# Kernel optimization log

Hardware: AMD Instinct MI355X
Metric: run time of the kernel (lower is better)

## Reference

```python
import jax, jax.numpy as jnp
import numpy as np

N = 100000   # nodes
E = 800000   # edges
IN = 64      # in_channels
H = 128      # hidden_channels (Embedding_Dimension)
K = 9        # Num_TCN clusters
EPS = 1e-15


def setup_inputs() -> dict:
    key = jax.random.key(0)
    k0, k1, k2, k3, k4 = jax.random.split(key, 5)
    x = jax.random.normal(k0, (N, IN), jnp.float32)
    edge_index = jax.random.randint(k1, (2, E), 0, N, dtype=jnp.int32)
    batch = jnp.zeros((N,), jnp.int32)  # single graph
    W1 = jax.random.normal(k2, (IN, H), jnp.float32) / np.sqrt(IN)
    b1 = jnp.zeros((H,), jnp.float32)
    Wp = jax.random.normal(k3, (H, K), jnp.float32) / np.sqrt(H)
    bp = jax.random.normal(k4, (K,), jnp.float32) * 0.01
    return {"x": x, "edge_index": edge_index, "batch": batch,
            "W1": W1, "b1": b1, "Wp": Wp, "bp": bp}


def gcn_conv(x, edge_index, W, b):
    # GCNConv: h = D^{-1/2} (A + I) D^{-1/2} (x W) + b
    n = x.shape[0]
    h = x @ W  # [N, H]
    loop = jnp.arange(n, dtype=edge_index.dtype)
    row = jnp.concatenate([edge_index[0], loop])  # source
    col = jnp.concatenate([edge_index[1], loop])  # target
    deg = jax.ops.segment_sum(jnp.ones_like(col, jnp.float32), col, n)
    dinv = jax.lax.rsqrt(jnp.maximum(deg, 1.0))  # deg >= 1 (self loops)
    norm = dinv[row] * dinv[col]  # [E+N]
    agg = jax.ops.segment_sum(norm[:, None] * h[row], col, n)  # scatter-add at targets
    return agg + b


def reference(x, edge_index, batch, W1, b1, Wp, bp):
    n = x.shape[0]
    src, dst = edge_index[0], edge_index[1]

    hx = jax.nn.relu(gcn_conv(x, edge_index, W1, b1))  # [N, H]
    s_logits = hx @ Wp + bp                             # [N, K]
    s = jax.nn.softmax(s_logits, axis=-1)

    # pooled features and adjacency: S^T X, S^T A S (A sparse via edge list)
    x_pool = s.T @ hx                                   # [K, H]
    out_adj = jnp.einsum('ek,el->kl', s[src], s[dst])   # [K, K]

    # mincut loss: -Tr(S^T A S) / Tr(S^T D S)
    mincut_num = jnp.trace(out_adj)
    deg_a = jax.ops.segment_sum(jnp.ones((src.shape[0],), jnp.float32), dst, n)
    mincut_den = jnp.sum(deg_a * jnp.sum(s * s, axis=-1))
    mc = -(mincut_num / (mincut_den + EPS))

    # orthogonality loss: || S^T S / ||S^T S||_F - I/sqrt(K) ||_F
    ss = s.T @ s
    o = jnp.linalg.norm(ss / jnp.linalg.norm(ss) - jnp.eye(K, dtype=s.dtype) / jnp.sqrt(jnp.float32(K)))

    # normalize pooled adjacency: zero diag, symmetric degree normalization
    oa = out_adj * (1.0 - jnp.eye(K, dtype=out_adj.dtype))
    d = jnp.sum(oa, axis=-1)
    dis = jax.lax.rsqrt(d + EPS)
    oa = dis[:, None] * oa * dis[None, :]

    out = jax.nn.log_softmax(x_pool[None], axis=-1)     # [1, K, H]
    return out, mc, o, s, oa[None]
```

## Files before the change

kernel.cpp:

```cpp
#include <hip/hip_runtime.h>
#include <hip/hip_bf16.h>

#define NN 100000
#define NE 800000
#define INC 64
#define HID 128
#define KC 9
#define NBKT 782
#define BCAP 2048
#define LDA 72
#define LDH 132

#define G_XP 0
#define G_OA 1152
#define G_SS 1233
#define G_DEN 1314

typedef __attribute__((ext_vector_type(8))) short bfrag;
typedef __attribute__((ext_vector_type(4))) float facc4;

__device__ __forceinline__ float atomAddG(float* p, float v) {
  return unsafeAtomicAdd(p, v);
}

__device__ __forceinline__ unsigned short bf16rn(float x) {
  unsigned u = __float_as_uint(x);
  return (unsigned short)((u + 0x7fffu + ((u >> 16) & 1u)) >> 16);
}

__device__ __forceinline__ float bf2f(unsigned s) {
  return __uint_as_float(s << 16);
}

__device__ __forceinline__ void acc8(float wt, uint4 rv, float* acc) {
  acc[0] = fmaf(wt, bf2f(rv.x & 0xffffu), acc[0]);
  acc[1] = fmaf(wt, bf2f(rv.x >> 16), acc[1]);
  acc[2] = fmaf(wt, bf2f(rv.y & 0xffffu), acc[2]);
  acc[3] = fmaf(wt, bf2f(rv.y >> 16), acc[3]);
  acc[4] = fmaf(wt, bf2f(rv.z & 0xffffu), acc[4]);
  acc[5] = fmaf(wt, bf2f(rv.z >> 16), acc[5]);
  acc[6] = fmaf(wt, bf2f(rv.w & 0xffffu), acc[6]);
  acc[7] = fmaf(wt, bf2f(rv.w >> 16), acc[7]);
}


__global__ __launch_bounds__(256) void k_binA(const int* __restrict__ src, const int* __restrict__ dst,
                                              const float* __restrict__ W1, const float* __restrict__ Wp,
                                              const float* __restrict__ x,
                                              int* __restrict__ bcur, int* __restrict__ ebuf,
                                              unsigned short* __restrict__ W1Thi,
                                              unsigned short* __restrict__ W1Tlo,
                                              float* __restrict__ wpsT,
                                              unsigned short* __restrict__ xb) {
  int t = threadIdx.x;
  if (blockIdx.x >= 129) {
    int idx = (blockIdx.x - 129) * 256 + t;
    for (int i = idx; i < NN * 8; i += 64 * 256) {
      float4 a = ((const float4*)x)[2 * i];
      float4 b = ((const float4*)x)[2 * i + 1];
      uint4 o;
      o.x = (unsigned)bf16rn(a.x) | ((unsigned)bf16rn(a.y) << 16);
      o.y = (unsigned)bf16rn(a.z) | ((unsigned)bf16rn(a.w) << 16);
      o.z = (unsigned)bf16rn(b.x) | ((unsigned)bf16rn(b.y) << 16);
      o.w = (unsigned)bf16rn(b.z) | ((unsigned)bf16rn(b.w) << 16);
      ((uint4*)xb)[i] = o;
    }
    return;
  }
  if (blockIdx.x == 128) {
    for (int i = t; i < (INC * HID) / 4; i += 256) {
      int k = i >> 5, c4 = (i & 31) * 4;
      float4 v = ((const float4*)W1)[i];
      float vv[4] = {v.x, v.y, v.z, v.w};
#pragma unroll
      for (int j = 0; j < 4; ++j) {
        unsigned short h = bf16rn(vv[j]);
        float lo = vv[j] - __uint_as_float((unsigned)h << 16);
        W1Thi[(c4 + j) * 64 + k] = h;
        W1Tlo[(c4 + j) * 64 + k] = bf16rn(lo);
      }
    }
    for (int i = t; i < KC * HID; i += 256) {
      int q = i >> 7, c = i & 127;
      wpsT[i] = Wp[c * KC + q];
    }
    return;
  }
  __shared__ int hist[NBKT];
  __shared__ int hbase[NBKT];
  for (int b = t; b < NBKT; b += 256) hist[b] = 0;
  __syncthreads();
  int beg = blockIdx.x * 6250, end = beg + 6250;
  for (int i = beg + t; i < end; i += 256) atomicAdd(&hist[dst[i] >> 7], 1);
  __syncthreads();
  for (int b = t; b < NBKT; b += 256) {
    int h = hist[b];
    hbase[b] = h ? atomicAdd(&bcur[b], h) : 0;
    hist[b] = 0;
  }
  __syncthreads();
  for (int i = beg + t; i < end; i += 256) {
    int d = dst[i], s = src[i];
    int b = d >> 7;
    int r = atomicAdd(&hist[b], 1);
    ebuf[(size_t)b * BCAP + hbase[b] + r] = s | ((d & 127) << 17);
  }
}

__global__ __launch_bounds__(256) void k_scanb(const int* __restrict__ bcur, int* __restrict__ bbase) {
  __shared__ int sc[1024];
  int t = threadIdx.x;
  for (int i = t; i < 1024; i += 256) sc[i] = (i < NBKT) ? bcur[i] : 0;
  __syncthreads();
  for (int off = 1; off < 1024; off <<= 1) {
    int v0 = (t >= off) ? sc[t - off] : 0;
    int v1 = (t + 256 >= off) ? sc[t + 256 - off] : 0;
    int v2 = (t + 512 >= off) ? sc[t + 512 - off] : 0;
    int v3 = (t + 768 >= off) ? sc[t + 768 - off] : 0;
    __syncthreads();
    sc[t] += v0; sc[t + 256] += v1; sc[t + 512] += v2; sc[t + 768] += v3;
    __syncthreads();
  }
  for (int i = t; i < NBKT; i += 256) bbase[i] = sc[i] - bcur[i];
}

__global__ __launch_bounds__(256) void k_fillB(const int* __restrict__ bcur, const int* __restrict__ bbase,
                                               const int* __restrict__ ebuf, int* __restrict__ rowptr,
                                               int* __restrict__ degi, float* __restrict__ dinv,
                                               int* __restrict__ csr) {
  __shared__ int cnt[128], loc[128], lcur[128];
  int b = blockIdx.x;
  int t = threadIdx.x;
  if (t < 128) cnt[t] = 0;
  __syncthreads();
  int n = bcur[b];
  const int* eb = ebuf + (size_t)b * BCAP;
  for (int i = t; i < n; i += 256) atomicAdd(&cnt[eb[i] >> 17], 1);
  __syncthreads();
  if (t < 128) loc[t] = cnt[t];
  __syncthreads();
  for (int off = 1; off < 128; off <<= 1) {
    int u = (t >= off && t < 128) ? loc[t - off] : 0;
    __syncthreads();
    if (t < 128) loc[t] += u;
    __syncthreads();
  }
  int gbase = bbase[b];
  if (t < 128) {
    int node = (b << 7) + t;
    int rp = gbase + loc[t] - cnt[t];
    if (node < NN) {
      rowptr[node] = rp;
      degi[node] = cnt[t];
      dinv[node] = rsqrtf((float)cnt[t] + 1.f);
    }
    lcur[t] = rp;
  }
  __syncthreads();
  for (int i = t; i < n; i += 256) {
    int pack = eb[i];
    int s = pack & 0x1FFFF;
    int dl = pack >> 17;
    int p = atomicAdd(&lcur[dl], 1);
    csr[p] = s;
  }
}


__global__ __launch_bounds__(256) void k_gather(const int* __restrict__ rowptr, const int* __restrict__ degi,
                                                const int* __restrict__ csr,
                                                const unsigned short* __restrict__ xb,
                                                const float* __restrict__ dinv, float* __restrict__ agg) {
  int t = threadIdx.x;
  int wave = t >> 6, lane = t & 63;
  int gw = blockIdx.x * 4 + wave;
  int ng = lane >> 3, c8 = lane & 7;
  int node = gw * 8 + ng;
  if (node >= NN) return;

  float dv = dinv[node];
  int base = rowptr[node];
  int cnt = degi[node];

  float acc[8];
  {
    uint4 v = *(const uint4*)(xb + (size_t)node * 64 + c8 * 8);
    float dv2 = dv * dv;
    acc[0] = dv2 * bf2f(v.x & 0xffffu); acc[1] = dv2 * bf2f(v.x >> 16);
    acc[2] = dv2 * bf2f(v.y & 0xffffu); acc[3] = dv2 * bf2f(v.y >> 16);
    acc[4] = dv2 * bf2f(v.z & 0xffffu); acc[5] = dv2 * bf2f(v.z >> 16);
    acc[6] = dv2 * bf2f(v.w & 0xffffu); acc[7] = dv2 * bf2f(v.w >> 16);
  }

  int j = 0;
  for (; j + 3 < cnt; j += 4) {
    int s0 = csr[base + j], s1 = csr[base + j + 1], s2 = csr[base + j + 2], s3 = csr[base + j + 3];
    float w0 = dinv[s0] * dv, w1 = dinv[s1] * dv, w2 = dinv[s2] * dv, w3 = dinv[s3] * dv;
    uint4 r0 = *(const uint4*)(xb + (size_t)s0 * 64 + c8 * 8);
    uint4 r1 = *(const uint4*)(xb + (size_t)s1 * 64 + c8 * 8);
    uint4 r2 = *(const uint4*)(xb + (size_t)s2 * 64 + c8 * 8);
    uint4 r3 = *(const uint4*)(xb + (size_t)s3 * 64 + c8 * 8);
    acc8(w0, r0, acc);
    acc8(w1, r1, acc);
    acc8(w2, r2, acc);
    acc8(w3, r3, acc);
  }
  for (; j < cnt; ++j) {
    int si = csr[base + j];
    float wq = dinv[si] * dv;
    uint4 rq = *(const uint4*)(xb + (size_t)si * 64 + c8 * 8);
    acc8(wq, rq, acc);
  }
  float* ao = agg + (size_t)node * INC + c8 * 8;
  *(float4*)ao = make_float4(acc[0], acc[1], acc[2], acc[3]);
  *(float4*)(ao + 4) = make_float4(acc[4], acc[5], acc[6], acc[7]);
}


__global__ __launch_bounds__(256, 2) void k_mlpA(const float* __restrict__ agg,
                                                 const unsigned short* __restrict__ W1Thi,
                                                 const unsigned short* __restrict__ W1Tlo,
                                                 const float* __restrict__ wpsT_g,
                                                 const float* __restrict__ b1, const float* __restrict__ bp,
                                                 float* __restrict__ s_out, float* __restrict__ s_pad,
                                                 float* __restrict__ pool_part) {
  __shared__ char smem[78336];
  short* Ahi = (short*)smem;
  short* Alo = Ahi + 128 * LDA;
  short* Whi = Alo + 128 * LDA;
  short* Wlo = Whi + 128 * LDA;
  float* Hs = (float*)smem;
  float* s_lds = Hs + 128 * LDH;
  float* wpsT = (float*)(smem + 73728);

  int t = threadIdx.x;
  int nbase = blockIdx.x * 128;

#pragma unroll
  for (int j = 0; j < 8; ++j) {
    int task = t + 256 * j;
    int n = task >> 4, kq = (task & 15) * 4;
    float4 v = make_float4(0.f, 0.f, 0.f, 0.f);
    if (nbase + n < NN) v = *(const float4*)(agg + (size_t)(nbase + n) * INC + kq);
    unsigned short h0 = bf16rn(v.x), h1 = bf16rn(v.y), h2 = bf16rn(v.z), h3 = bf16rn(v.w);
    float l0f = v.x - __uint_as_float((unsigned)h0 << 16);
    float l1f = v.y - __uint_as_float((unsigned)h1 << 16);
    float l2f = v.z - __uint_as_float((unsigned)h2 << 16);
    float l3f = v.w - __uint_as_float((unsigned)h3 << 16);
    unsigned short q0 = bf16rn(l0f), q1 = bf16rn(l1f), q2 = bf16rn(l2f), q3 = bf16rn(l3f);
    *(uint2*)&Ahi[n * LDA + kq] = make_uint2((unsigned)h0 | ((unsigned)h1 << 16),
                                             (unsigned)h2 | ((unsigned)h3 << 16));
    *(uint2*)&Alo[n * LDA + kq] = make_uint2((unsigned)q0 | ((unsigned)q1 << 16),
                                             (unsigned)q2 | ((unsigned)q3 << 16));
  }
#pragma unroll
  for (int j = 0; j < 8; ++j) {
    int task = t + 256 * j;
    int c = task >> 4, k4 = (task & 15) * 4;
    *(uint2*)&Whi[c * LDA + k4] = *(const uint2*)&W1Thi[c * 64 + k4];
    *(uint2*)&Wlo[c * LDA + k4] = *(const uint2*)&W1Tlo[c * 64 + k4];
  }
  for (int i = t; i < KC * HID; i += 256) wpsT[i] = wpsT_g[i];
  __syncthreads();

  int w = t >> 6, l = t & 63;
  int r0 = w * 32;
  int lrow = l & 15;
  int lk = (l >> 4) * 8;
  int rg = (l >> 4) * 4;

  facc4 acc[2][8];
#pragma unroll
  for (int mt = 0; mt < 2; ++mt)
#pragma unroll
    for (int nt = 0; nt < 8; ++nt) acc[mt][nt] = (facc4){0.f, 0.f, 0.f, 0.f};

#pragma unroll
  for (int ks = 0; ks < 2; ++ks) {
    int ko = ks * 32 + lk;
    bfrag a0h = *(const bfrag*)&Ahi[(r0 + lrow) * LDA + ko];
    bfrag a0l = *(const bfrag*)&Alo[(r0 + lrow) * LDA + ko];
    bfrag a1h = *(const bfrag*)&Ahi[(r0 + 16 + lrow) * LDA + ko];
    bfrag a1l = *(const bfrag*)&Alo[(r0 + 16 + lrow) * LDA + ko];
#pragma unroll
    for (int nt = 0; nt < 8; ++nt) {
      bfrag bh = *(const bfrag*)&Whi[(nt * 16 + lrow) * LDA + ko];
      bfrag bl = *(const bfrag*)&Wlo[(nt * 16 + lrow) * LDA + ko];
      acc[0][nt] = __builtin_amdgcn_mfma_f32_16x16x32_bf16(a0l, bh, acc[0][nt], 0, 0, 0);
      acc[0][nt] = __builtin_amdgcn_mfma_f32_16x16x32_bf16(a0h, bl, acc[0][nt], 0, 0, 0);
      acc[0][nt] = __builtin_amdgcn_mfma_f32_16x16x32_bf16(a0h, bh, acc[0][nt], 0, 0, 0);
      acc[1][nt] = __builtin_amdgcn_mfma_f32_16x16x32_bf16(a1l, bh, acc[1][nt], 0, 0, 0);
      acc[1][nt] = __builtin_amdgcn_mfma_f32_16x16x32_bf16(a1h, bl, acc[1][nt], 0, 0, 0);
      acc[1][nt] = __builtin_amdgcn_mfma_f32_16x16x32_bf16(a1h, bh, acc[1][nt], 0, 0, 0);
    }
  }
  __syncthreads();

#pragma unroll
  for (int nt = 0; nt < 8; ++nt) {
    float b1v = b1[nt * 16 + lrow];
#pragma unroll
    for (int mt = 0; mt < 2; ++mt)
#pragma unroll
      for (int r = 0; r < 4; ++r)
        Hs[(r0 + mt * 16 + rg + r) * LDH + nt * 16 + lrow] =
            fmaxf(acc[mt][nt][r] + b1v, 0.f);
  }
  __syncthreads();

  {
    int node = t >> 1, half = t & 1;
    const float4* hrow = (const float4*)(Hs + node * LDH + half * 64);
    float4 h4[16];
#pragma unroll
    for (int cc = 0; cc < 16; ++cc) h4[cc] = hrow[cc];

    float lg[KC];
#pragma unroll
    for (int q = 0; q < KC; ++q) {
      const float4* w4 = (const float4*)(wpsT + q * HID + half * 64);
      float s0 = 0.f, s1 = 0.f, s2 = 0.f, s3 = 0.f;
#pragma unroll
      for (int cc = 0; cc < 16; ++cc) {
        float4 wv = w4[cc];
        s0 = fmaf(h4[cc].x, wv.x, s0);
        s1 = fmaf(h4[cc].y, wv.y, s1);
        s2 = fmaf(h4[cc].z, wv.z, s2);
        s3 = fmaf(h4[cc].w, wv.w, s3);
      }
      lg[q] = (s0 + s1) + (s2 + s3);
    }
#pragma unroll
    for (int q = 0; q < KC; ++q)
      lg[q] = lg[q] + __shfl_xor(lg[q], 1, 64) + bp[q];

    float m = lg[0];
#pragma unroll
    for (int q = 1; q < KC; ++q) m = fmaxf(m, lg[q]);
    float Z = 0.f;
#pragma unroll
    for (int q = 0; q < KC; ++q) { lg[q] = __expf(lg[q] - m); Z += lg[q]; }
    float inv = 1.0f / Z;
#pragma unroll
    for (int q = 0; q < KC; ++q) lg[q] *= inv;

    float4* sl = (float4*)(s_lds + node * 12);
    int gnode = nbase + node;
    if (half == 0) {
      sl[0] = make_float4(lg[0], lg[1], lg[2], lg[3]);
      if (gnode < NN) {
        ((float4*)(s_pad + (size_t)gnode * 12))[0] = make_float4(lg[0], lg[1], lg[2], lg[3]);
        float* so = s_out + (size_t)gnode * KC;
        so[0] = lg[0]; so[1] = lg[1]; so[2] = lg[2]; so[3] = lg[3]; so[4] = lg[4];
      }
    } else {
      sl[1] = make_float4(lg[4], lg[5], lg[6], lg[7]);
      s_lds[node * 12 + 8] = lg[8];
      if (gnode < NN) {
        ((float4*)(s_pad + (size_t)gnode * 12))[1] = make_float4(lg[4], lg[5], lg[6], lg[7]);
        ((float4*)(s_pad + (size_t)gnode * 12))[2] = make_float4(lg[8], 0.f, 0.f, 0.f);
        float* so = s_out + (size_t)gnode * KC;
        so[5] = lg[5]; so[6] = lg[6]; so[7] = lg[7]; so[8] = lg[8];
      }
    }
  }
  __syncthreads();

  {
    int c = t & 127, nh = t >> 7;
    float pool[KC];
#pragma unroll
    for (int q = 0; q < KC; ++q) pool[q] = 0.f;
    int lim = NN - nbase - nh * 64;
    if (lim > 64) lim = 64;
    for (int i = 0; i < lim; ++i) {
      int node = nh * 64 + i;
      float4 sa = *(const float4*)(s_lds + node * 12);
      float4 sb = *(const float4*)(s_lds + node * 12 + 4);
      float s8 = s_lds[node * 12 + 8];
      float h = Hs[node * LDH + c];
      pool[0] = fmaf(sa.x, h, pool[0]);
      pool[1] = fmaf(sa.y, h, pool[1]);
      pool[2] = fmaf(sa.z, h, pool[2]);
      pool[3] = fmaf(sa.w, h, pool[3]);
      pool[4] = fmaf(sb.x, h, pool[4]);
      pool[5] = fmaf(sb.y, h, pool[5]);
      pool[6] = fmaf(sb.z, h, pool[6]);
      pool[7] = fmaf(sb.w, h, pool[7]);
      pool[8] = fmaf(s8, h, pool[8]);
    }
    float* pp = pool_part + (size_t)(blockIdx.x * 2 + nh) * (KC * HID);
#pragma unroll
    for (int q = 0; q < KC; ++q) pp[q * HID + c] = pool[q];
  }
}


__global__ __launch_bounds__(256) void k_ssden(const float* __restrict__ s_pad,
                                               const int* __restrict__ degi,
                                               const float* __restrict__ pool_part,
                                               float* __restrict__ glob) {
  int t = threadIdx.x;
  int tid = blockIdx.x * 256 + t;
  int stride = gridDim.x * 256;

  {
    float a0 = 0.f, a1 = 0.f, a2 = 0.f, a3 = 0.f, a4 = 0.f;
    for (int p = blockIdx.x; p < 2 * NBKT; p += gridDim.x) {
      const float* row = pool_part + (size_t)p * (KC * HID);
      a0 += row[t];
      a1 += row[t + 256];
      a2 += row[t + 512];
      a3 += row[t + 768];
      if (t < 128) a4 += row[t + 1024];
    }
    atomAddG(&glob[G_XP + t], a0);
    atomAddG(&glob[G_XP + t + 256], a1);
    atomAddG(&glob[G_XP + t + 512], a2);
    atomAddG(&glob[G_XP + t + 768], a3);
    if (t < 128) atomAddG(&glob[G_XP + t + 1024], a4);
  }

  float acc[81];
  float den = 0.f;
#pragma unroll
  for (int i = 0; i < 81; ++i) acc[i] = 0.f;

  for (int node = tid; node < NN; node += stride) {
    const float4* sn = (const float4*)(s_pad + (size_t)node * 12);
    float4 a = sn[0], b = sn[1], c = sn[2];
    float s[9] = {a.x, a.y, a.z, a.w, b.x, b.y, b.z, b.w, c.x};
    float dg = (float)degi[node];
    float nrm = 0.f;
#pragma unroll
    for (int i = 0; i < 9; ++i) nrm = fmaf(s[i], s[i], nrm);
    den = fmaf(dg, nrm, den);
#pragma unroll
    for (int i = 0; i < 9; ++i)
#pragma unroll
      for (int j = 0; j < 9; ++j) acc[i * 9 + j] = fmaf(s[i], s[j], acc[i * 9 + j]);
  }

  __shared__ float wsum[4][82];
#pragma unroll
  for (int i = 0; i < 81; ++i) {
#pragma unroll
    for (int off = 32; off > 0; off >>= 1) acc[i] += __shfl_xor(acc[i], off, 64);
  }
#pragma unroll
  for (int off = 32; off > 0; off >>= 1) den += __shfl_xor(den, off, 64);
  int wave = t >> 6, lane = t & 63;
  if (lane == 0) {
#pragma unroll
    for (int i = 0; i < 81; ++i) wsum[wave][i] = acc[i];
    wsum[wave][81] = den;
  }
  __syncthreads();
  if (t < 81) atomAddG(&glob[G_SS + t], wsum[0][t] + wsum[1][t] + wsum[2][t] + wsum[3][t]);
  if (t == 81) atomAddG(&glob[G_DEN], wsum[0][81] + wsum[1][81] + wsum[2][81] + wsum[3][81]);
}


__global__ __launch_bounds__(256) void k_adj(const int* __restrict__ rowptr, const int* __restrict__ degi,
                                             const int* __restrict__ csr, const float* __restrict__ s_pad,
                                             float* __restrict__ oa_g) {
  int t = threadIdx.x;
  int tid = blockIdx.x * blockDim.x + t;
  int stride = gridDim.x * blockDim.x;

  float acc[81];
#pragma unroll
  for (int i = 0; i < 81; ++i) acc[i] = 0.f;

  for (int node = tid; node < NN; node += stride) {
    int base = rowptr[node];
    int cnt = degi[node];
    float4 g0 = make_float4(0.f, 0.f, 0.f, 0.f);
    float4 g1 = g0;
    float g8 = 0.f;
    int j = 0;
    for (; j + 1 < cnt; j += 2) {
      int s0 = csr[base + j], s1 = csr[base + j + 1];
      const float4* p0 = (const float4*)(s_pad + (size_t)s0 * 12);
      const float4* p1 = (const float4*)(s_pad + (size_t)s1 * 12);
      float4 a0 = p0[0], b0 = p0[1], c0 = p0[2];
      float4 a1 = p1[0], b1 = p1[1], c1 = p1[2];
      g0.x += a0.x + a1.x; g0.y += a0.y + a1.y; g0.z += a0.z + a1.z; g0.w += a0.w + a1.w;
      g1.x += b0.x + b1.x; g1.y += b0.y + b1.y; g1.z += b0.z + b1.z; g1.w += b0.w + b1.w;
      g8 += c0.x + c1.x;
    }
    if (j < cnt) {
      int s0 = csr[base + j];
      const float4* p0 = (const float4*)(s_pad + (size_t)s0 * 12);
      float4 a0 = p0[0], b0 = p0[1], c0 = p0[2];
      g0.x += a0.x; g0.y += a0.y; g0.z += a0.z; g0.w += a0.w;
      g1.x += b0.x; g1.y += b0.y; g1.z += b0.z; g1.w += b0.w;
      g8 += c0.x;
    }
    const float4* sn = (const float4*)(s_pad + (size_t)node * 12);
    float4 d0 = sn[0], d1 = sn[1], d2 = sn[2];
    float gg[9] = {g0.x, g0.y, g0.z, g0.w, g1.x, g1.y, g1.z, g1.w, g8};
    float sd[9] = {d0.x, d0.y, d0.z, d0.w, d1.x, d1.y, d1.z, d1.w, d2.x};
#pragma unroll
    for (int i = 0; i < 9; ++i)
#pragma unroll
      for (int jj = 0; jj < 9; ++jj) acc[i * 9 + jj] = fmaf(gg[i], sd[jj], acc[i * 9 + jj]);
  }

  __shared__ float wsum[4][81];
#pragma unroll
  for (int i = 0; i < 81; ++i) {
#pragma unroll
    for (int off = 32; off > 0; off >>= 1) acc[i] += __shfl_xor(acc[i], off, 64);
  }
  int wave = t >> 6, lane = t & 63;
  if (lane == 0) {
#pragma unroll
    for (int i = 0; i < 81; ++i) wsum[wave][i] = acc[i];
  }
  __syncthreads();
  if (t < 81) atomAddG(&oa_g[t], wsum[0][t] + wsum[1][t] + wsum[2][t] + wsum[3][t]);
}


__global__ __launch_bounds__(128) void k_final(const float* __restrict__ glob, float* __restrict__ out) {
  const float* xp = glob + G_XP;
  const float* oa = glob + G_OA;
  const float* ssm = glob + G_SS;
  const float* den = glob + G_DEN;
  int t = threadIdx.x;
  __shared__ float red[128];

  for (int k = 0; k < 9; ++k) {
    float v = xp[k * 128 + t];
    red[t] = v;
    __syncthreads();
    for (int s2 = 64; s2 > 0; s2 >>= 1) {
      if (t < s2) red[t] = fmaxf(red[t], red[t + s2]);
      __syncthreads();
    }
    float m = red[0];
    __syncthreads();
    red[t] = expf(v - m);
    __syncthreads();
    for (int s2 = 64; s2 > 0; s2 >>= 1) {
      if (t < s2) red[t] += red[t + s2];
      __syncthreads();
    }
    float lz = logf(red[0]) + m;
    __syncthreads();
    out[k * 128 + t] = v - lz;
  }

  if (t == 0) {
    float num = 0.f;
    for (int q = 0; q < 9; ++q) num += oa[q * 9 + q];
    out[1152] = -(num / (den[0] + 1e-15f));

    float fn = 0.f;
    for (int i = 0; i < 81; ++i) fn += ssm[i] * ssm[i];
    float rfn = 1.0f / sqrtf(fn);
    float osum = 0.f;
    for (int i = 0; i < 9; ++i)
      for (int j = 0; j < 9; ++j) {
        float v = ssm[i * 9 + j] * rfn - ((i == j) ? (1.0f / 3.0f) : 0.f);
        osum += v * v;
      }
    out[1153] = sqrtf(osum);
  }

  __shared__ float dsh[9];
  if (t < 9) {
    float d = 0.f;
    for (int j = 0; j < 9; ++j)
      if (j != t) d += oa[t * 9 + j];
    dsh[t] = 1.0f / sqrtf(d + 1e-15f);
  }
  __syncthreads();
  if (t < 81) {
    int i = t / 9, j = t % 9;
    out[901154 + t] = (i == j) ? 0.f : dsh[i] * oa[t] * dsh[j];
  }
}

extern "C" void kernel_launch(void* const* d_in, const int* in_sizes, int n_in,
                              void* d_out, int out_size, void* d_ws, size_t ws_size,
                              hipStream_t stream) {
  const float* x = (const float*)d_in[0];
  const int* ei = (const int*)d_in[1];
  const float* W1 = (const float*)d_in[3];
  const float* b1 = (const float*)d_in[4];
  const float* Wp = (const float*)d_in[5];
  const float* bp = (const float*)d_in[6];
  float* out = (float*)d_out;

  float* glob = (float*)d_ws;
  int* bcur = (int*)d_ws + 1316;
  int* bbase = (int*)d_ws + 2116;
  int* rowptr = (int*)d_ws + 2944;
  int* degi = rowptr + NN;
  int* csr = degi + NN;
  float* dinv = (float*)(csr + NE);
  float* s_pad = dinv + NN;
  float* agg = s_pad + (size_t)NN * 12;
  int* ebuf = (int*)(agg + (size_t)NN * INC);
  float* pool_part = (float*)(ebuf + (size_t)NBKT * BCAP);
  unsigned short* W1Thi = (unsigned short*)(pool_part + (size_t)NBKT * 2 * (KC * HID));
  unsigned short* W1Tlo = W1Thi + INC * HID;
  float* wpsT = (float*)(W1Tlo + INC * HID);
  unsigned short* xb = (unsigned short*)(wpsT + KC * HID);

  hipMemsetAsync(d_ws, 0, (size_t)2116 * sizeof(float), stream);

  const int* src = ei;
  const int* dst = ei + NE;

  hipLaunchKernelGGL(k_binA, dim3(193), dim3(256), 0, stream, src, dst, W1, Wp, x,
                     bcur, ebuf, W1Thi, W1Tlo, wpsT, xb);
  hipLaunchKernelGGL(k_scanb, dim3(1), dim3(256), 0, stream, bcur, bbase);
  hipLaunchKernelGGL(k_fillB, dim3(NBKT), dim3(256), 0, stream, bcur, bbase, ebuf,
                     rowptr, degi, dinv, csr);
  hipLaunchKernelGGL(k_gather, dim3((NN + 31) / 32), dim3(256), 0, stream,
                     rowptr, degi, csr, xb, dinv, agg);
  hipLaunchKernelGGL(k_mlpA, dim3(NBKT), dim3(256), 0, stream, agg,
                     W1Thi, W1Tlo, wpsT, b1, bp, out + 1154, s_pad, pool_part);
  hipLaunchKernelGGL(k_ssden, dim3(128), dim3(256), 0, stream, s_pad, degi, pool_part, glob);
  hipLaunchKernelGGL(k_adj, dim3(1024), dim3(256), 0, stream, rowptr, degi, csr, s_pad, glob + G_OA);
  hipLaunchKernelGGL(k_final, dim3(1), dim3(128), 0, stream, glob, out);
}
```

Measured before the change: 236.3 us.

## Halve MLP block tile to 64 nodes and read weights directly from global

The fused MLP/softmax/pool kernel now handles 64 nodes per block instead of 128, which roughly halves LDS use and doubles the grid. The launch bound is raised so four blocks can share a CU. W1 and Wp fragments are no longer staged in LDS and are read straight from global memory or cache. In exchange, weight traffic per node rises, half the threads sit idle in the logits phase, and there are twice as many pooled partials for the reduction kernel to sum.

```diff
diff --git a/kernel.cpp b/kernel.cpp
--- a/kernel.cpp
+++ b/kernel.cpp
@@ -7,6 +7,7 @@
 #define HID 128
 #define KC 9
 #define NBKT 782
+#define NB2 1563
 #define BCAP 2048
 #define LDA 72
 #define LDH 132
@@ -217,27 +218,24 @@
 }
 
 
-__global__ __launch_bounds__(256, 2) void k_mlpA(const float* __restrict__ agg,
+__global__ __launch_bounds__(256, 4) void k_mlpA(const float* __restrict__ agg,
                                                  const unsigned short* __restrict__ W1Thi,
                                                  const unsigned short* __restrict__ W1Tlo,
                                                  const float* __restrict__ wpsT_g,
                                                  const float* __restrict__ b1, const float* __restrict__ bp,
                                                  float* __restrict__ s_out, float* __restrict__ s_pad,
                                                  float* __restrict__ pool_part) {
-  __shared__ char smem[78336];
+  __shared__ char smem[36864];
   short* Ahi = (short*)smem;
-  short* Alo = Ahi + 128 * LDA;
-  short* Whi = Alo + 128 * LDA;
-  short* Wlo = Whi + 128 * LDA;
+  short* Alo = Ahi + 64 * LDA;
   float* Hs = (float*)smem;
-  float* s_lds = Hs + 128 * LDH;
-  float* wpsT = (float*)(smem + 73728);
-
-  int t = threadIdx.x;
-  int nbase = blockIdx.x * 128;
-
-#pragma unroll
-  for (int j = 0; j < 8; ++j) {
+  float* s_lds = Hs + 64 * LDH;
+
+  int t = threadIdx.x;
+  int nbase = blockIdx.x * 64;
+
+#pragma unroll
+  for (int j = 0; j < 4; ++j) {
     int task = t + 256 * j;
     int n = task >> 4, kq = (task & 15) * 4;
     float4 v = make_float4(0.f, 0.f, 0.f, 0.f);
@@ -253,45 +251,30 @@
     *(uint2*)&Alo[n * LDA + kq] = make_uint2((unsigned)q0 | ((unsigned)q1 << 16),
                                              (unsigned)q2 | ((unsigned)q3 << 16));
   }
-#pragma unroll
-  for (int j = 0; j < 8; ++j) {
-    int task = t + 256 * j;
-    int c = task >> 4, k4 = (task & 15) * 4;
-    *(uint2*)&Whi[c * LDA + k4] = *(const uint2*)&W1Thi[c * 64 + k4];
-    *(uint2*)&Wlo[c * LDA + k4] = *(const uint2*)&W1Tlo[c * 64 + k4];
-  }
-  for (int i = t; i < KC * HID; i += 256) wpsT[i] = wpsT_g[i];
   __syncthreads();
 
   int w = t >> 6, l = t & 63;
-  int r0 = w * 32;
+  int r0 = w * 16;
   int lrow = l & 15;
   int lk = (l >> 4) * 8;
   int rg = (l >> 4) * 4;
 
-  facc4 acc[2][8];
-#pragma unroll
-  for (int mt = 0; mt < 2; ++mt)
-#pragma unroll
-    for (int nt = 0; nt < 8; ++nt) acc[mt][nt] = (facc4){0.f, 0.f, 0.f, 0.f};
+  facc4 acc[8];
+#pragma unroll
+  for (int nt = 0; nt < 8; ++nt) acc[nt] = (facc4){0.f, 0.f, 0.f, 0.f};
 
 #pragma unroll
   for (int ks = 0; ks < 2; ++ks) {
     int ko = ks * 32 + lk;
-    bfrag a0h = *(const bfrag*)&Ahi[(r0 + lrow) * LDA + ko];
-    bfrag a0l = *(const bfrag*)&Alo[(r0 + lrow) * LDA + ko];
-    bfrag a1h = *(const bfrag*)&Ahi[(r0 + 16 + lrow) * LDA + ko];
-    bfrag a1l = *(const bfrag*)&Alo[(r0 + 16 + lrow) * LDA + ko];
+    bfrag ah = *(const bfrag*)&Ahi[(r0 + lrow) * LDA + ko];
+    bfrag al = *(const bfrag*)&Alo[(r0 + lrow) * LDA + ko];
 #pragma unroll
     for (int nt = 0; nt < 8; ++nt) {
-      bfrag bh = *(const bfrag*)&Whi[(nt * 16 + lrow) * LDA + ko];
-      bfrag bl = *(const bfrag*)&Wlo[(nt * 16 + lrow) * LDA + ko];
-      acc[0][nt] = __builtin_amdgcn_mfma_f32_16x16x32_bf16(a0l, bh, acc[0][nt], 0, 0, 0);
-      acc[0][nt] = __builtin_amdgcn_mfma_f32_16x16x32_bf16(a0h, bl, acc[0][nt], 0, 0, 0);
-      acc[0][nt] = __builtin_amdgcn_mfma_f32_16x16x32_bf16(a0h, bh, acc[0][nt], 0, 0, 0);
-      acc[1][nt] = __builtin_amdgcn_mfma_f32_16x16x32_bf16(a1l, bh, acc[1][nt], 0, 0, 0);
-      acc[1][nt] = __builtin_amdgcn_mfma_f32_16x16x32_bf16(a1h, bl, acc[1][nt], 0, 0, 0);
-      acc[1][nt] = __builtin_amdgcn_mfma_f32_16x16x32_bf16(a1h, bh, acc[1][nt], 0, 0, 0);
+      bfrag bh = *(const bfrag*)&W1Thi[(nt * 16 + lrow) * 64 + ko];
+      bfrag bl = *(const bfrag*)&W1Tlo[(nt * 16 + lrow) * 64 + ko];
+      acc[nt] = __builtin_amdgcn_mfma_f32_16x16x32_bf16(al, bh, acc[nt], 0, 0, 0);
+      acc[nt] = __builtin_amdgcn_mfma_f32_16x16x32_bf16(ah, bl, acc[nt], 0, 0, 0);
+      acc[nt] = __builtin_amdgcn_mfma_f32_16x16x32_bf16(ah, bh, acc[nt], 0, 0, 0);
     }
   }
   __syncthreads();
@@ -300,15 +283,12 @@
   for (int nt = 0; nt < 8; ++nt) {
     float b1v = b1[nt * 16 + lrow];
 #pragma unroll
-    for (int mt = 0; mt < 2; ++mt)
-#pragma unroll
-      for (int r = 0; r < 4; ++r)
-        Hs[(r0 + mt * 16 + rg + r) * LDH + nt * 16 + lrow] =
-            fmaxf(acc[mt][nt][r] + b1v, 0.f);
-  }
-  __syncthreads();
-
-  {
+    for (int r = 0; r < 4; ++r)
+      Hs[(r0 + rg + r) * LDH + nt * 16 + lrow] = fmaxf(acc[nt][r] + b1v, 0.f);
+  }
+  __syncthreads();
+
+  if (t < 128) {
     int node = t >> 1, half = t & 1;
     const float4* hrow = (const float4*)(Hs + node * LDH + half * 64);
     float4 h4[16];
@@ -318,7 +298,7 @@
     float lg[KC];
 #pragma unroll
     for (int q = 0; q < KC; ++q) {
-      const float4* w4 = (const float4*)(wpsT + q * HID + half * 64);
+      const float4* w4 = (const float4*)(wpsT_g + q * HID + half * 64);
       float s0 = 0.f, s1 = 0.f, s2 = 0.f, s3 = 0.f;
 #pragma unroll
       for (int cc = 0; cc < 16; ++cc) {
@@ -367,14 +347,14 @@
   __syncthreads();
 
   {
-    int c = t & 127, nh = t >> 7;
+    int c = t & 127, set = t >> 7;
     float pool[KC];
 #pragma unroll
     for (int q = 0; q < KC; ++q) pool[q] = 0.f;
-    int lim = NN - nbase - nh * 64;
-    if (lim > 64) lim = 64;
+    int lim = NN - nbase - set * 32;
+    if (lim > 32) lim = 32;
     for (int i = 0; i < lim; ++i) {
-      int node = nh * 64 + i;
+      int node = set * 32 + i;
       float4 sa = *(const float4*)(s_lds + node * 12);
       float4 sb = *(const float4*)(s_lds + node * 12 + 4);
       float s8 = s_lds[node * 12 + 8];
@@ -389,7 +369,7 @@
       pool[7] = fmaf(sb.w, h, pool[7]);
       pool[8] = fmaf(s8, h, pool[8]);
     }
-    float* pp = pool_part + (size_t)(blockIdx.x * 2 + nh) * (KC * HID);
+    float* pp = pool_part + (size_t)(blockIdx.x * 2 + set) * (KC * HID);
 #pragma unroll
     for (int q = 0; q < KC; ++q) pp[q * HID + c] = pool[q];
   }
@@ -406,7 +386,7 @@
 
   {
     float a0 = 0.f, a1 = 0.f, a2 = 0.f, a3 = 0.f, a4 = 0.f;
-    for (int p = blockIdx.x; p < 2 * NBKT; p += gridDim.x) {
+    for (int p = blockIdx.x; p < 2 * NB2; p += gridDim.x) {
       const float* row = pool_part + (size_t)p * (KC * HID);
       a0 += row[t];
       a1 += row[t + 256];
@@ -605,7 +585,7 @@
   float* agg = s_pad + (size_t)NN * 12;
   int* ebuf = (int*)(agg + (size_t)NN * INC);
   float* pool_part = (float*)(ebuf + (size_t)NBKT * BCAP);
-  unsigned short* W1Thi = (unsigned short*)(pool_part + (size_t)NBKT * 2 * (KC * HID));
+  unsigned short* W1Thi = (unsigned short*)(pool_part + (size_t)NB2 * 2 * (KC * HID));
   unsigned short* W1Tlo = W1Thi + INC * HID;
   float* wpsT = (float*)(W1Tlo + INC * HID);
   unsigned short* xb = (unsigned short*)(wpsT + KC * HID);
@@ -622,7 +602,7 @@
                      rowptr, degi, dinv, csr);
   hipLaunchKernelGGL(k_gather, dim3((NN + 31) / 32), dim3(256), 0, stream,
                      rowptr, degi, csr, xb, dinv, agg);
-  hipLaunchKernelGGL(k_mlpA, dim3(NBKT), dim3(256), 0, stream, agg,
+  hipLaunchKernelGGL(k_mlpA, dim3(NB2), dim3(256), 0, stream, agg,
                      W1Thi, W1Tlo, wpsT, b1, bp, out + 1154, s_pad, pool_part);
   hipLaunchKernelGGL(k_ssden, dim3(128), dim3(256), 0, stream, s_pad, degi, pool_part, glob);
   hipLaunchKernelGGL(k_adj, dim3(1024), dim3(256), 0, stream, rowptr, degi, csr, s_pad, glob + G_OA);
```

Result: slower. 269.5 us (+14.0%).

## Store gather output as pre-split bf16 MFMA fragments and shrink MLP LDS

Applied to the files above, without the earlier changes.

The gather kernel now writes its aggregated features directly as hi/lo bf16 pairs in the MFMA fragment tile layout, so the MLP kernel loads A fragments straight from global memory. This removes the fp32 agg round trip, the split/convert step and the LDS staging of A. The hidden activations are stored in LDS as bf16 instead of fp32, which cuts shared memory enough to raise occupancy to 3 blocks per CU. Storing hidden activations in bf16 adds rounding error to the softmax logits and pooled features, and an extra k_binA block zeroes the padded tail tiles.

```diff
diff --git a/kernel.cpp b/kernel.cpp
--- a/kernel.cpp
+++ b/kernel.cpp
@@ -9,7 +9,8 @@
 #define NBKT 782
 #define BCAP 2048
 #define LDA 72
-#define LDH 132
+#define LDH2 132
+#define NTIL 6256
 
 #define G_XP 0
 #define G_OA 1152
@@ -51,8 +52,16 @@
                                               unsigned short* __restrict__ W1Thi,
                                               unsigned short* __restrict__ W1Tlo,
                                               float* __restrict__ wpsT,
-                                              unsigned short* __restrict__ xb) {
-  int t = threadIdx.x;
+                                              unsigned short* __restrict__ xb,
+                                              unsigned short* __restrict__ aggF_hi,
+                                              unsigned short* __restrict__ aggF_lo) {
+  int t = threadIdx.x;
+  if (blockIdx.x == 193) {
+    unsigned* ph = (unsigned*)(aggF_hi + (size_t)6250 * 1024);
+    unsigned* pl = (unsigned*)(aggF_lo + (size_t)6250 * 1024);
+    for (int i = t; i < 3072; i += 256) { ph[i] = 0u; pl[i] = 0u; }
+    return;
+  }
   if (blockIdx.x >= 129) {
     int idx = (blockIdx.x - 129) * 256 + t;
     for (int i = idx; i < NN * 8; i += 64 * 256) {
@@ -170,7 +179,9 @@
 __global__ __launch_bounds__(256) void k_gather(const int* __restrict__ rowptr, const int* __restrict__ degi,
                                                 const int* __restrict__ csr,
                                                 const unsigned short* __restrict__ xb,
-                                                const float* __restrict__ dinv, float* __restrict__ agg) {
+                                                const float* __restrict__ dinv,
+                                                unsigned short* __restrict__ aggF_hi,
+                                                unsigned short* __restrict__ aggF_lo) {
   int t = threadIdx.x;
   int wave = t >> 6, lane = t & 63;
   int gw = blockIdx.x * 4 + wave;
@@ -211,48 +222,48 @@
     uint4 rq = *(const uint4*)(xb + (size_t)si * 64 + c8 * 8);
     acc8(wq, rq, acc);
   }
-  float* ao = agg + (size_t)node * INC + c8 * 8;
-  *(float4*)ao = make_float4(acc[0], acc[1], acc[2], acc[3]);
-  *(float4*)(ao + 4) = make_float4(acc[4], acc[5], acc[6], acc[7]);
-}
-
-
-__global__ __launch_bounds__(256, 2) void k_mlpA(const float* __restrict__ agg,
+
+  unsigned short hs[8], ls[8];
+#pragma unroll
+  for (int i = 0; i < 8; ++i) {
+    hs[i] = bf16rn(acc[i]);
+    ls[i] = bf16rn(acc[i] - __uint_as_float((unsigned)hs[i] << 16));
+  }
+  int tile = node >> 4, lrow = node & 15;
+  int ks = c8 >> 2, kgrp = c8 & 3;
+  size_t off = ((size_t)(tile * 2 + ks)) * 512 + (kgrp * 16 + lrow) * 8;
+  uint4 ho, lo;
+  ho.x = (unsigned)hs[0] | ((unsigned)hs[1] << 16);
+  ho.y = (unsigned)hs[2] | ((unsigned)hs[3] << 16);
+  ho.z = (unsigned)hs[4] | ((unsigned)hs[5] << 16);
+  ho.w = (unsigned)hs[6] | ((unsigned)hs[7] << 16);
+  lo.x = (unsigned)ls[0] | ((unsigned)ls[1] << 16);
+  lo.y = (unsigned)ls[2] | ((unsigned)ls[3] << 16);
+  lo.z = (unsigned)ls[4] | ((unsigned)ls[5] << 16);
+  lo.w = (unsigned)ls[6] | ((unsigned)ls[7] << 16);
+  *(uint4*)(aggF_hi + off) = ho;
+  *(uint4*)(aggF_lo + off) = lo;
+}
+
+
+__global__ __launch_bounds__(256, 3) void k_mlpA(const unsigned short* __restrict__ aggF_hi,
+                                                 const unsigned short* __restrict__ aggF_lo,
                                                  const unsigned short* __restrict__ W1Thi,
                                                  const unsigned short* __restrict__ W1Tlo,
                                                  const float* __restrict__ wpsT_g,
                                                  const float* __restrict__ b1, const float* __restrict__ bp,
                                                  float* __restrict__ s_out, float* __restrict__ s_pad,
                                                  float* __restrict__ pool_part) {
-  __shared__ char smem[78336];
-  short* Ahi = (short*)smem;
-  short* Alo = Ahi + 128 * LDA;
-  short* Whi = Alo + 128 * LDA;
+  __shared__ char smem[47616];
+  short* Whi = (short*)smem;
   short* Wlo = Whi + 128 * LDA;
-  float* Hs = (float*)smem;
-  float* s_lds = Hs + 128 * LDH;
-  float* wpsT = (float*)(smem + 73728);
+  short* Hbf = (short*)smem;
+  float* s_lds = (float*)(smem + 36864);
+  float* wpsT = (float*)(smem + 43008);
 
   int t = threadIdx.x;
   int nbase = blockIdx.x * 128;
 
-#pragma unroll
-  for (int j = 0; j < 8; ++j) {
-    int task = t + 256 * j;
-    int n = task >> 4, kq = (task & 15) * 4;
-    float4 v = make_float4(0.f, 0.f, 0.f, 0.f);
-    if (nbase + n < NN) v = *(const float4*)(agg + (size_t)(nbase + n) * INC + kq);
-    unsigned short h0 = bf16rn(v.x), h1 = bf16rn(v.y), h2 = bf16rn(v.z), h3 = bf16rn(v.w);
-    float l0f = v.x - __uint_as_float((unsigned)h0 << 16);
-    float l1f = v.y - __uint_as_float((unsigned)h1 << 16);
-    float l2f = v.z - __uint_as_float((unsigned)h2 << 16);
-    float l3f = v.w - __uint_as_float((unsigned)h3 << 16);
-    unsigned short q0 = bf16rn(l0f), q1 = bf16rn(l1f), q2 = bf16rn(l2f), q3 = bf16rn(l3f);
-    *(uint2*)&Ahi[n * LDA + kq] = make_uint2((unsigned)h0 | ((unsigned)h1 << 16),
-                                             (unsigned)h2 | ((unsigned)h3 << 16));
-    *(uint2*)&Alo[n * LDA + kq] = make_uint2((unsigned)q0 | ((unsigned)q1 << 16),
-                                             (unsigned)q2 | ((unsigned)q3 << 16));
-  }
 #pragma unroll
   for (int j = 0; j < 8; ++j) {
     int task = t + 256 * j;
@@ -266,8 +277,19 @@
   int w = t >> 6, l = t & 63;
   int r0 = w * 32;
   int lrow = l & 15;
-  int lk = (l >> 4) * 8;
   int rg = (l >> 4) * 4;
+  int tg0 = blockIdx.x * 8 + 2 * w;
+
+  bfrag a0h[2], a0l[2], a1h[2], a1l[2];
+#pragma unroll
+  for (int ks = 0; ks < 2; ++ks) {
+    size_t o0 = ((size_t)(tg0 * 2 + ks)) * 512 + l * 8;
+    size_t o1 = ((size_t)((tg0 + 1) * 2 + ks)) * 512 + l * 8;
+    a0h[ks] = *(const bfrag*)(aggF_hi + o0);
+    a0l[ks] = *(const bfrag*)(aggF_lo + o0);
+    a1h[ks] = *(const bfrag*)(aggF_hi + o1);
+    a1l[ks] = *(const bfrag*)(aggF_lo + o1);
+  }
 
   facc4 acc[2][8];
 #pragma unroll
@@ -277,21 +299,17 @@
 
 #pragma unroll
   for (int ks = 0; ks < 2; ++ks) {
-    int ko = ks * 32 + lk;
-    bfrag a0h = *(const bfrag*)&Ahi[(r0 + lrow) * LDA + ko];
-    bfrag a0l = *(const bfrag*)&Alo[(r0 + lrow) * LDA + ko];
-    bfrag a1h = *(const bfrag*)&Ahi[(r0 + 16 + lrow) * LDA + ko];
-    bfrag a1l = *(const bfrag*)&Alo[(r0 + 16 + lrow) * LDA + ko];
+    int ko = ks * 32 + (l >> 4) * 8;
 #pragma unroll
     for (int nt = 0; nt < 8; ++nt) {
       bfrag bh = *(const bfrag*)&Whi[(nt * 16 + lrow) * LDA + ko];
       bfrag bl = *(const bfrag*)&Wlo[(nt * 16 + lrow) * LDA + ko];
-      acc[0][nt] = __builtin_amdgcn_mfma_f32_16x16x32_bf16(a0l, bh, acc[0][nt], 0, 0, 0);
-      acc[0][nt] = __builtin_amdgcn_mfma_f32_16x16x32_bf16(a0h, bl, acc[0][nt], 0, 0, 0);
-      acc[0][nt] = __builtin_amdgcn_mfma_f32_16x16x32_bf16(a0h, bh, acc[0][nt], 0, 0, 0);
-      acc[1][nt] = __builtin_amdgcn_mfma_f32_16x16x32_bf16(a1l, bh, acc[1][nt], 0, 0, 0);
-      acc[1][nt] = __builtin_amdgcn_mfma_f32_16x16x32_bf16(a1h, bl, acc[1][nt], 0, 0, 0);
-      acc[1][nt] = __builtin_amdgcn_mfma_f32_16x16x32_bf16(a1h, bh, acc[1][nt], 0, 0, 0);
+      acc[0][nt] = __builtin_amdgcn_mfma_f32_16x16x32_bf16(a0l[ks], bh, acc[0][nt], 0, 0, 0);
+      acc[0][nt] = __builtin_amdgcn_mfma_f32_16x16x32_bf16(a0h[ks], bl, acc[0][nt], 0, 0, 0);
+      acc[0][nt] = __builtin_amdgcn_mfma_f32_16x16x32_bf16(a0h[ks], bh, acc[0][nt], 0, 0, 0);
+      acc[1][nt] = __builtin_amdgcn_mfma_f32_16x16x32_bf16(a1l[ks], bh, acc[1][nt], 0, 0, 0);
+      acc[1][nt] = __builtin_amdgcn_mfma_f32_16x16x32_bf16(a1h[ks], bl, acc[1][nt], 0, 0, 0);
+      acc[1][nt] = __builtin_amdgcn_mfma_f32_16x16x32_bf16(a1h[ks], bh, acc[1][nt], 0, 0, 0);
     }
   }
   __syncthreads();
@@ -302,18 +320,25 @@
 #pragma unroll
     for (int mt = 0; mt < 2; ++mt)
 #pragma unroll
-      for (int r = 0; r < 4; ++r)
-        Hs[(r0 + mt * 16 + rg + r) * LDH + nt * 16 + lrow] =
-            fmaxf(acc[mt][nt][r] + b1v, 0.f);
+      for (int r = 0; r < 4; ++r) {
+        float h = fmaxf(acc[mt][nt][r] + b1v, 0.f);
+        Hbf[(r0 + mt * 16 + rg + r) * LDH2 + nt * 16 + lrow] = (short)bf16rn(h);
+      }
   }
   __syncthreads();
 
   {
     int node = t >> 1, half = t & 1;
-    const float4* hrow = (const float4*)(Hs + node * LDH + half * 64);
-    float4 h4[16];
-#pragma unroll
-    for (int cc = 0; cc < 16; ++cc) h4[cc] = hrow[cc];
+    const short* hr = Hbf + node * LDH2 + half * 64;
+    float hv[64];
+#pragma unroll
+    for (int cc = 0; cc < 16; ++cc) {
+      uint2 uh = *(const uint2*)(hr + cc * 4);
+      hv[4 * cc + 0] = bf2f(uh.x & 0xffffu);
+      hv[4 * cc + 1] = bf2f(uh.x >> 16);
+      hv[4 * cc + 2] = bf2f(uh.y & 0xffffu);
+      hv[4 * cc + 3] = bf2f(uh.y >> 16);
+    }
 
     float lg[KC];
 #pragma unroll
@@ -323,10 +348,10 @@
 #pragma unroll
       for (int cc = 0; cc < 16; ++cc) {
         float4 wv = w4[cc];
-        s0 = fmaf(h4[cc].x, wv.x, s0);
-        s1 = fmaf(h4[cc].y, wv.y, s1);
-        s2 = fmaf(h4[cc].z, wv.z, s2);
-        s3 = fmaf(h4[cc].w, wv.w, s3);
+        s0 = fmaf(hv[4 * cc + 0], wv.x, s0);
+        s1 = fmaf(hv[4 * cc + 1], wv.y, s1);
+        s2 = fmaf(hv[4 * cc + 2], wv.z, s2);
+        s3 = fmaf(hv[4 * cc + 3], wv.w, s3);
       }
       lg[q] = (s0 + s1) + (s2 + s3);
     }
@@ -378,7 +403,7 @@
       float4 sa = *(const float4*)(s_lds + node * 12);
       float4 sb = *(const float4*)(s_lds + node * 12 + 4);
       float s8 = s_lds[node * 12 + 8];
-      float h = Hs[node * LDH + c];
+      float h = bf2f((unsigned short)Hbf[node * LDH2 + c]);
       pool[0] = fmaf(sa.x, h, pool[0]);
       pool[1] = fmaf(sa.y, h, pool[1]);
       pool[2] = fmaf(sa.z, h, pool[2]);
@@ -602,8 +627,9 @@
   int* csr = degi + NN;
   float* dinv = (float*)(csr + NE);
   float* s_pad = dinv + NN;
-  float* agg = s_pad + (size_t)NN * 12;
-  int* ebuf = (int*)(agg + (size_t)NN * INC);
+  unsigned short* aggF_hi = (unsigned short*)(s_pad + (size_t)NN * 12);
+  unsigned short* aggF_lo = aggF_hi + (size_t)NTIL * 1024;
+  int* ebuf = (int*)(aggF_lo + (size_t)NTIL * 1024);
   float* pool_part = (float*)(ebuf + (size_t)NBKT * BCAP);
   unsigned short* W1Thi = (unsigned short*)(pool_part + (size_t)NBKT * 2 * (KC * HID));
   unsigned short* W1Tlo = W1Thi + INC * HID;
@@ -615,14 +641,14 @@
   const int* src = ei;
   const int* dst = ei + NE;
 
-  hipLaunchKernelGGL(k_binA, dim3(193), dim3(256), 0, stream, src, dst, W1, Wp, x,
-                     bcur, ebuf, W1Thi, W1Tlo, wpsT, xb);
+  hipLaunchKernelGGL(k_binA, dim3(194), dim3(256), 0, stream, src, dst, W1, Wp, x,
+                     bcur, ebuf, W1Thi, W1Tlo, wpsT, xb, aggF_hi, aggF_lo);
   hipLaunchKernelGGL(k_scanb, dim3(1), dim3(256), 0, stream, bcur, bbase);
   hipLaunchKernelGGL(k_fillB, dim3(NBKT), dim3(256), 0, stream, bcur, bbase, ebuf,
                      rowptr, degi, dinv, csr);
   hipLaunchKernelGGL(k_gather, dim3((NN + 31) / 32), dim3(256), 0, stream,
-                     rowptr, degi, csr, xb, dinv, agg);
-  hipLaunchKernelGGL(k_mlpA, dim3(NBKT), dim3(256), 0, stream, agg,
+                     rowptr, degi, csr, xb, dinv, aggF_hi, aggF_lo);
+  hipLaunchKernelGGL(k_mlpA, dim3(NBKT), dim3(256), 0, stream, aggF_hi, aggF_lo,
                      W1Thi, W1Tlo, wpsT, b1, bp, out + 1154, s_pad, pool_part);
   hipLaunchKernelGGL(k_ssden, dim3(128), dim3(256), 0, stream, s_pad, degi, pool_part, glob);
   hipLaunchKernelGGL(k_adj, dim3(1024), dim3(256), 0, stream, rowptr, degi, csr, s_pad, glob + G_OA);
```

Result: slower. 373.4 us (+58.0%).
